# Kernel tuning notes

Hardware: AMD Instinct MI355X
Metric: run time of the kernel (lower is better)

The kernel has to match this reference:

```python
import jax, jax.numpy as jnp
import numpy as np

N_NODES = 50000
N_EDGES = 800000
D = 128


def setup_inputs() -> dict:
    key = jax.random.key(0)
    k1, k2, k3, k4, k5 = jax.random.split(key, 5)
    N = jax.random.normal(k1, (N_NODES, D), dtype=jnp.float32)
    W1 = jax.random.normal(k2, (D, D), dtype=jnp.float32) * (1.0 / np.sqrt(D))
    w2 = jax.random.normal(k3, (D,), dtype=jnp.float32) * (1.0 / np.sqrt(D))
    src = jax.random.randint(k4, (N_EDGES,), 0, N_NODES, dtype=jnp.int32)
    dst = jax.random.randint(k5, (N_EDGES,), 0, N_NODES, dtype=jnp.int32)
    return {"N": N, "W1": W1, "w2": w2, "src": src, "dst": dst}


def reference(N, W1, w2, src, dst):
    n_nodes = N.shape[0]
    # Per-node attention logit: fc2(tanh(fc1(N))). Logit depends only on the
    # source node, so compute once per node then gather per edge (same math).
    logit = jnp.tanh(N @ W1.T) @ w2            # [n_nodes]
    e = logit[src]                              # [n_edges] per-edge logit
    # Segment softmax over each destination node's incoming edges
    seg_max = jax.ops.segment_max(e, dst, num_segments=n_nodes)
    seg_max = jnp.where(jnp.isfinite(seg_max), seg_max, 0.0)  # empty segments
    ex = jnp.exp(e - seg_max[dst])              # [n_edges]
    denom = jax.ops.segment_sum(ex, dst, num_segments=n_nodes)  # [n_nodes]
    a = ex / denom[dst]                         # attention weight per edge
    # Weighted scatter-sum of gathered source features
    Np = jax.ops.segment_sum(a[:, None] * N[src], dst, num_segments=n_nodes)
    return Np
```

## Files before the change

kernel.cpp:

```cpp
#include <hip/hip_runtime.h>
#include <hip/hip_bf16.h>

#define D 128
#define NPB 16
#define CHUNK 6144
#define BKN 64
#define MAXBUCK 1024
#define NCHUNK_MAX 192
#define CAP 4096

typedef __attribute__((ext_vector_type(8))) short bf16x8;
typedef __attribute__((ext_vector_type(4))) float f32x4;

__device__ __forceinline__ unsigned short f2bf_rne(float f) {
  unsigned u = __float_as_uint(f);
  unsigned r = (u + 0x7FFFu + ((u >> 16) & 1u)) >> 16;
  return (unsigned short)r;
}

__device__ __forceinline__ float fast_tanh(float x) {
  float e = __expf(2.0f * x);
  return 1.0f - 2.0f / (e + 1.0f);
}

__device__ __forceinline__ void split8(const float* __restrict__ p,
                                       bf16x8& hv, bf16x8& lv) {
  float4 a = *(const float4*)p;
  float4 b = *(const float4*)(p + 4);
  float xs[8] = {a.x, a.y, a.z, a.w, b.x, b.y, b.z, b.w};
#pragma unroll
  for (int i = 0; i < 8; ++i) {
    unsigned short h = f2bf_rne(xs[i]);
    float hf = __uint_as_float((unsigned)h << 16);
    hv[i] = (short)h;
    lv[i] = (short)f2bf_rne(xs[i] - hf);
  }
}

struct SMLogit {
  unsigned short lhi[64 * 128];
  unsigned short llo[64 * 128];
  float part[4][64];
};
struct SMBin {
  unsigned cnt[MAXBUCK];
  unsigned cur[MAXBUCK];
  unsigned ebuf[CHUNK];
  int sdata[256];
};
union SMU {
  SMLogit lg;
  SMBin bn;
};

__global__ __launch_bounds__(256, 2) void logit_bin_kernel(
    const float* __restrict__ Nm, const float* __restrict__ W1,
    const float* __restrict__ w2, float* __restrict__ explog,
    unsigned short* __restrict__ nbf, int n_nodes,
    const int* __restrict__ src, const int* __restrict__ dst,
    unsigned* __restrict__ binout, unsigned short* __restrict__ dir,
    int n_edges, int nbuck, int nblk_bin) {
  __shared__ SMU sm;
  const int tid = threadIdx.x;

  if ((int)blockIdx.x < nblk_bin) {
    const int blk = (int)blockIdx.x;
    const int ebase = blk * CHUNK;
    const int chunkN = min(CHUNK, n_edges - ebase);

    for (int i = tid; i < MAXBUCK; i += 256) sm.bn.cnt[i] = 0;
    __syncthreads();

    for (int i = tid; i < chunkN; i += 256) {
      int d = dst[ebase + i];
      atomicAdd(&sm.bn.cnt[d >> 6], 1u);
    }
    __syncthreads();

    int t4 = tid * 4;
    int c0 = sm.bn.cnt[t4], c1 = sm.bn.cnt[t4 + 1];
    int c2 = sm.bn.cnt[t4 + 2], c3 = sm.bn.cnt[t4 + 3];
    int s = c0 + c1 + c2 + c3;
    sm.bn.sdata[tid] = s;
    __syncthreads();
    for (int d = 1; d < 256; d <<= 1) {
      int v = (tid >= d) ? sm.bn.sdata[tid - d] : 0;
      __syncthreads();
      sm.bn.sdata[tid] += v;
      __syncthreads();
    }
    int tb = sm.bn.sdata[tid] - s;
    sm.bn.cur[t4] = tb;
    sm.bn.cur[t4 + 1] = tb + c0;
    sm.bn.cur[t4 + 2] = tb + c0 + c1;
    sm.bn.cur[t4 + 3] = tb + c0 + c1 + c2;
    __syncthreads();

    size_t dbase = (size_t)blk * (nbuck + 1);
    for (int k = tid; k < nbuck; k += 256)
      dir[dbase + k] = (unsigned short)sm.bn.cur[k];
    if (tid == 0) dir[dbase + nbuck] = (unsigned short)chunkN;
    __syncthreads();

    for (int i = tid; i < chunkN; i += 256) {
      int d = dst[ebase + i];
      int sv = src[ebase + i];
      unsigned slot = atomicAdd(&sm.bn.cur[d >> 6], 1u);
      sm.bn.ebuf[slot] = (unsigned)sv | ((unsigned)(d & 63) << 16);
    }
    __syncthreads();

    for (int i = tid; i < chunkN; i += 256) binout[ebase + i] = sm.bn.ebuf[i];
  } else {
    const int w = tid >> 6;
    const int l = tid & 63;
    const int lg = l >> 4;
    const int ln = l & 15;
    const int base = ((int)blockIdx.x - nblk_bin) * 64;

    bf16x8 Bh[2][4], Bl[2][4];
#pragma unroll
    for (int ntl = 0; ntl < 2; ++ntl) {
      int n = (w * 2 + ntl) * 16 + ln;
#pragma unroll
      for (int kt = 0; kt < 4; ++kt) {
        int k = kt * 32 + lg * 8;
        split8(W1 + n * 128 + k, Bh[ntl][kt], Bl[ntl][kt]);
      }
    }

#pragma unroll
    for (int i = 0; i < 8; ++i) {
      int flat = tid + i * 256;
      int row = flat >> 5;
      int c4 = flat & 31;
      int grow = base + row;
      if (grow >= n_nodes) grow = n_nodes - 1;
      float4 v = *(const float4*)(Nm + (size_t)grow * D + c4 * 4);
      unsigned short h0 = f2bf_rne(v.x), h1 = f2bf_rne(v.y);
      unsigned short h2 = f2bf_rne(v.z), h3 = f2bf_rne(v.w);
      unsigned short o0 = f2bf_rne(v.x - __uint_as_float((unsigned)h0 << 16));
      unsigned short o1 = f2bf_rne(v.y - __uint_as_float((unsigned)h1 << 16));
      unsigned short o2 = f2bf_rne(v.z - __uint_as_float((unsigned)h2 << 16));
      unsigned short o3 = f2bf_rne(v.w - __uint_as_float((unsigned)h3 << 16));
      int boff = (c4 * 8) ^ ((row & 7) << 4);
      *(ushort4*)((char*)sm.lg.lhi + row * 256 + boff) =
          make_ushort4(h0, h1, h2, h3);
      *(ushort4*)((char*)sm.lg.llo + row * 256 + boff) =
          make_ushort4(o0, o1, o2, o3);
      *(ushort4*)(nbf + (size_t)grow * D + c4 * 4) =
          make_ushort4(h0, h1, h2, h3);
    }
    __syncthreads();

    f32x4 acc[4][2];
#pragma unroll
    for (int mt = 0; mt < 4; ++mt)
#pragma unroll
      for (int ntl = 0; ntl < 2; ++ntl)
        acc[mt][ntl] = (f32x4){0.f, 0.f, 0.f, 0.f};

#pragma unroll
    for (int mt = 0; mt < 4; ++mt) {
      int row = mt * 16 + ln;
      bf16x8 Ah[4], Al[4];
#pragma unroll
      for (int kt = 0; kt < 4; ++kt) {
        int boff = (kt * 64 + lg * 16) ^ ((row & 7) << 4);
        Ah[kt] = *(const bf16x8*)((const char*)sm.lg.lhi + row * 256 + boff);
        Al[kt] = *(const bf16x8*)((const char*)sm.lg.llo + row * 256 + boff);
      }
#pragma unroll
      for (int ntl = 0; ntl < 2; ++ntl) {
#pragma unroll
        for (int kt = 0; kt < 4; ++kt) {
          acc[mt][ntl] = __builtin_amdgcn_mfma_f32_16x16x32_bf16(
              Ah[kt], Bh[ntl][kt], acc[mt][ntl], 0, 0, 0);
          acc[mt][ntl] = __builtin_amdgcn_mfma_f32_16x16x32_bf16(
              Ah[kt], Bl[ntl][kt], acc[mt][ntl], 0, 0, 0);
          acc[mt][ntl] = __builtin_amdgcn_mfma_f32_16x16x32_bf16(
              Al[kt], Bh[ntl][kt], acc[mt][ntl], 0, 0, 0);
        }
      }
    }

    float w2a = w2[(w * 2 + 0) * 16 + ln];
    float w2b = w2[(w * 2 + 1) * 16 + ln];
#pragma unroll
    for (int mt = 0; mt < 4; ++mt) {
      float s0 =
          fast_tanh(acc[mt][0][0]) * w2a + fast_tanh(acc[mt][1][0]) * w2b;
      float s1 =
          fast_tanh(acc[mt][0][1]) * w2a + fast_tanh(acc[mt][1][1]) * w2b;
      float s2 =
          fast_tanh(acc[mt][0][2]) * w2a + fast_tanh(acc[mt][1][2]) * w2b;
      float s3 =
          fast_tanh(acc[mt][0][3]) * w2a + fast_tanh(acc[mt][1][3]) * w2b;
#pragma unroll
      for (int mask = 1; mask < 16; mask <<= 1) {
        s0 += __shfl_xor(s0, mask);
        s1 += __shfl_xor(s1, mask);
        s2 += __shfl_xor(s2, mask);
        s3 += __shfl_xor(s3, mask);
      }
      if (ln < 4) {
        float sv = (ln == 0) ? s0 : (ln == 1) ? s1 : (ln == 2) ? s2 : s3;
        sm.lg.part[w][mt * 16 + lg * 4 + ln] = sv;
      }
    }
    __syncthreads();
    if (tid < 64) {
      int node = base + tid;
      if (node < n_nodes) {
        float t = sm.lg.part[0][tid] + sm.lg.part[1][tid] +
                  sm.lg.part[2][tid] + sm.lg.part[3][tid];
        explog[node] = expf(t);
      }
    }
  }
}

__global__ __launch_bounds__(256) void merge_kernel(
    const unsigned* __restrict__ binout, const unsigned short* __restrict__ dir,
    unsigned* __restrict__ sorted, int* __restrict__ offsets,
    int* __restrict__ ends, int n_nodes, int nbuck, int nblk_bin) {
  __shared__ unsigned ebuf[CAP];
  __shared__ int lens[NCHUNK_MAX], cstart[NCHUNK_MAX], ls0[NCHUNK_MAX];
  __shared__ int cnt[BKN], nstart[BKN], cur[BKN];
  __shared__ int total;
  const int tid = threadIdx.x;
  const int w = tid >> 6, lane = tid & 63;
  const int bk = blockIdx.x;
  const int node0 = bk * BKN;
  const int base = bk * CAP;

  if (tid < nblk_bin) {
    size_t dbase = (size_t)tid * (nbuck + 1);
    int s0 = dir[dbase + bk];
    int s1 = dir[dbase + bk + 1];
    ls0[tid] = s0;
    lens[tid] = s1 - s0;
  }
  if (tid < BKN) cnt[tid] = 0;
  __syncthreads();

  if (w == 0) {
    int l0 = lane * 3, l1 = l0 + 1, l2 = l0 + 2;
    int a = (l0 < nblk_bin) ? lens[l0] : 0;
    int b = (l1 < nblk_bin) ? lens[l1] : 0;
    int c = (l2 < nblk_bin) ? lens[l2] : 0;
    int sv = a + b + c;
    int inc = sv;
#pragma unroll
    for (int off = 1; off < 64; off <<= 1) {
      int t = __shfl_up(inc, off);
      if (lane >= off) inc += t;
    }
    int ex = inc - sv;
    if (l0 < nblk_bin) cstart[l0] = ex;
    if (l1 < nblk_bin) cstart[l1] = ex + a;
    if (l2 < nblk_bin) cstart[l2] = ex + a + b;
    if (lane == 63) total = (inc > CAP) ? CAP : inc;
  }
  __syncthreads();
  const int tot = total;

  for (int r = w; r < nblk_bin; r += 4) {
    int len = lens[r], cs = cstart[r];
    if (cs >= CAP) continue;
    if (cs + len > CAP) len = CAP - cs;
    const unsigned* g = binout + (size_t)r * CHUNK + ls0[r];
    for (int i = lane; i < len; i += 64) ebuf[cs + i] = g[i];
  }
  __syncthreads();

  for (int i = tid; i < tot; i += 256) atomicAdd(&cnt[ebuf[i] >> 16], 1);
  __syncthreads();

  if (w == 0) {
    int c = cnt[lane];
    int inc = c;
#pragma unroll
    for (int off = 1; off < 64; off <<= 1) {
      int t = __shfl_up(inc, off);
      if (lane >= off) inc += t;
    }
    nstart[lane] = inc - c;
  }
  __syncthreads();

  if (tid < BKN) {
    cur[tid] = nstart[tid];
    int node = node0 + tid;
    if (node < n_nodes) {
      offsets[node] = base + nstart[tid];
      ends[node] = base + nstart[tid] + cnt[tid];
    }
  }
  __syncthreads();

  for (int i = tid; i < tot; i += 256) {
    unsigned p = ebuf[i];
    int pos = atomicAdd(&cur[p >> 16], 1);
    sorted[(size_t)base + pos] = p;
  }
}

__global__ __launch_bounds__(256) void accum_sorted_kernel(
    const int* __restrict__ offsets, const int* __restrict__ ends,
    const unsigned* __restrict__ sorted, const float* __restrict__ explog,
    const unsigned short* __restrict__ nbf, float* __restrict__ out,
    int n_nodes) {
  int node = (blockIdx.x * 256 + threadIdx.x) >> 6;
  int lane = threadIdx.x & 63;
  if (node >= n_nodes) return;
  const int eg = lane >> 4;
  const int fl = lane & 15;
  int beg = offsets[node], end = ends[node];
  int last = end - 1;
  float acc[8];
#pragma unroll
  for (int j = 0; j < 8; ++j) acc[j] = 0.f;
  float den = 0.f;

  for (int e = beg; e < end; e += 8) {
    int ea = e + eg;
    int eb = e + 4 + eg;
    int eca = (ea < last) ? ea : last;
    int ecb = (eb < last) ? eb : last;
    unsigned pa = sorted[eca];
    unsigned pb = sorted[ecb];
    int sa = pa & 0xFFFF, sb = pb & 0xFFFF;
    float xa = explog[sa];
    float xb = explog[sb];
    uint4 ua = *(const uint4*)(nbf + (size_t)sa * D + fl * 8);
    uint4 ub = *(const uint4*)(nbf + (size_t)sb * D + fl * 8);
    xa = (ea < end) ? xa : 0.f;
    xb = (eb < end) ? xb : 0.f;
    den += xa + xb;
    unsigned va[4] = {ua.x, ua.y, ua.z, ua.w};
    unsigned vb[4] = {ub.x, ub.y, ub.z, ub.w};
#pragma unroll
    for (int j = 0; j < 4; ++j) {
      acc[2 * j] += xa * __uint_as_float(va[j] << 16) +
                    xb * __uint_as_float(vb[j] << 16);
      acc[2 * j + 1] += xa * __uint_as_float(va[j] & 0xFFFF0000u) +
                        xb * __uint_as_float(vb[j] & 0xFFFF0000u);
    }
  }

#pragma unroll
  for (int j = 0; j < 8; ++j) {
    acc[j] += __shfl_xor(acc[j], 16);
    acc[j] += __shfl_xor(acc[j], 32);
  }
  den += __shfl_xor(den, 16);
  den += __shfl_xor(den, 32);

  if (eg == 0) {
    float inv = (end > beg) ? 1.0f / den : 0.f;
    float4 o0 = make_float4(acc[0] * inv, acc[1] * inv, acc[2] * inv,
                            acc[3] * inv);
    float4 o1 = make_float4(acc[4] * inv, acc[5] * inv, acc[6] * inv,
                            acc[7] * inv);
    float* orow = out + (size_t)node * D + fl * 8;
    *(float4*)orow = o0;
    *(float4*)(orow + 4) = o1;
  }
}

__global__ __launch_bounds__(256) void logit_kernel(
    const float* __restrict__ Nm, const float* __restrict__ W1,
    const float* __restrict__ w2, float* __restrict__ logit, int n_nodes) {
  __shared__ float w1t[32 * 129];
  const int tid = threadIdx.x;
  const int j = tid & 127;
  const int half = tid >> 7;
  const int base = blockIdx.x * NPB;
  float acc[8];
#pragma unroll
  for (int g = 0; g < 8; ++g) acc[g] = 0.f;
  for (int c = 0; c < 4; ++c) {
    __syncthreads();
    for (int idx = tid; idx < 128 * 32; idx += 256) {
      int kl = idx & 31, jj = idx >> 5;
      w1t[kl * 129 + jj] = W1[jj * 128 + c * 32 + kl];
    }
    __syncthreads();
#pragma unroll
    for (int g = 0; g < 8; ++g) {
      int node = base + g * 2 + half;
      if (node < n_nodes) {
        const float4* nrow =
            reinterpret_cast<const float4*>(Nm + (size_t)node * D + c * 32);
        float a = acc[g];
#pragma unroll
        for (int k4 = 0; k4 < 8; ++k4) {
          float4 nv = nrow[k4];
          int kl = k4 * 4;
          a += nv.x * w1t[(kl + 0) * 129 + j];
          a += nv.y * w1t[(kl + 1) * 129 + j];
          a += nv.z * w1t[(kl + 2) * 129 + j];
          a += nv.w * w1t[(kl + 3) * 129 + j];
        }
        acc[g] = a;
      }
    }
  }
  const float w2j = w2[j];
#pragma unroll
  for (int g = 0; g < 8; ++g) {
    int node = base + g * 2 + half;
    float t = tanhf(acc[g]) * w2j;
#pragma unroll
    for (int off = 32; off; off >>= 1) t += __shfl_down(t, off);
    if ((tid & 63) == 0 && node < n_nodes) atomicAdd(&logit[node], t);
  }
}

__global__ __launch_bounds__(256) void denom_kernel(
    const int* __restrict__ src, const int* __restrict__ dst,
    const float* __restrict__ logit, float* __restrict__ denom, int n_edges) {
  int e = blockIdx.x * 256 + threadIdx.x;
  if (e < n_edges) {
    float ex = expf(logit[src[e]]);
    atomicAdd(&denom[dst[e]], ex);
  }
}

__global__ __launch_bounds__(256) void scatter_kernel(
    const int* __restrict__ src, const int* __restrict__ dst,
    const float* __restrict__ logit, const float* __restrict__ denom,
    const float* __restrict__ Nm, float* __restrict__ out, int n_edges) {
  int wave = (blockIdx.x * 256 + threadIdx.x) >> 6;
  int lane = threadIdx.x & 63;
  if (wave >= n_edges) return;
  int s = src[wave];
  int d = dst[wave];
  float a = expf(logit[s]) / denom[d];
  float v0 = Nm[(size_t)s * D + lane];
  float v1 = Nm[(size_t)s * D + 64 + lane];
  atomicAdd(&out[(size_t)d * D + lane], a * v0);
  atomicAdd(&out[(size_t)d * D + 64 + lane], a * v1);
}

static inline char* align_up(char* p, size_t a) {
  return (char*)(((uintptr_t)p + a - 1) & ~(uintptr_t)(a - 1));
}

extern "C" void kernel_launch(void* const* d_in, const int* in_sizes, int n_in,
                              void* d_out, int out_size, void* d_ws,
                              size_t ws_size, hipStream_t stream) {
  const float* Nm  = (const float*)d_in[0];
  const float* W1  = (const float*)d_in[1];
  const float* w2  = (const float*)d_in[2];
  const int*   src = (const int*)d_in[3];
  const int*   dst = (const int*)d_in[4];
  float* out = (float*)d_out;

  const int n_nodes = in_sizes[0] / D;
  const int n_edges = in_sizes[3];
  const int n_pad = (n_nodes + 63) & ~63;
  const int nbuck = (n_nodes + BKN - 1) / BKN;
  const int nblk_bin = (n_edges + CHUNK - 1) / CHUNK;

  char* p = (char*)d_ws;
  float* explog = (float*)p;     p = align_up(p + (size_t)n_pad * 4, 256);
  float* denomF = (float*)p;     p = align_up(p + (size_t)n_pad * 4, 256);
  unsigned short* nbf = (unsigned short*)p;
  p = align_up(p + (size_t)n_nodes * D * 2, 256);
  unsigned* binout = (unsigned*)p;
  p = align_up(p + (size_t)nblk_bin * CHUNK * 4, 256);
  unsigned short* dir = (unsigned short*)p;
  p = align_up(p + (size_t)nblk_bin * (nbuck + 1) * 2, 256);
  unsigned* sorted = (unsigned*)p;
  p = align_up(p + (size_t)nbuck * CAP * 4, 256);
  int* offsets = (int*)p;        p = align_up(p + (size_t)n_pad * 4, 256);
  int* ends    = (int*)p;        p = align_up(p + (size_t)n_pad * 4, 256);
  size_t needed = (size_t)(p - (char*)d_ws);

  const bool fits = (ws_size >= needed) && (n_nodes <= 65535) &&
                    (nbuck <= MAXBUCK) && (nblk_bin <= NCHUNK_MAX) &&
                    ((n_edges / (nbuck > 0 ? nbuck : 1)) * 3 < CAP);

  if (fits) {
    int nblk1 = (n_nodes + 63) / 64;
    logit_bin_kernel<<<nblk_bin + nblk1, 256, 0, stream>>>(
        Nm, W1, w2, explog, nbf, n_nodes, src, dst, binout, dir, n_edges,
        nbuck, nblk_bin);

    merge_kernel<<<nbuck, 256, 0, stream>>>(binout, dir, sorted, offsets,
                                            ends, n_nodes, nbuck, nblk_bin);

    int ablk = (n_nodes + 3) / 4;
    accum_sorted_kernel<<<ablk, 256, 0, stream>>>(
        offsets, ends, sorted, explog, nbf, out, n_nodes);
  } else {
    float* logit = explog;
    float* denom = denomF;
    hipMemsetAsync(logit, 0, (size_t)n_pad * sizeof(float), stream);
    hipMemsetAsync(denom, 0, (size_t)n_pad * sizeof(float), stream);
    hipMemsetAsync(out, 0, (size_t)out_size * sizeof(float), stream);
    int nblk1 = (n_nodes + NPB - 1) / NPB;
    logit_kernel<<<nblk1, 256, 0, stream>>>(Nm, W1, w2, logit, n_nodes);
    int eblk = (n_edges + 255) / 256;
    denom_kernel<<<eblk, 256, 0, stream>>>(src, dst, logit, denom, n_edges);
    int nblk3 = (n_edges + 3) / 4;
    scatter_kernel<<<nblk3, 256, 0, stream>>>(src, dst, logit, denom, Nm, out,
                                              n_edges);
  }
}
```

Baseline: 81.35 us.

## Shrink binning chunks, truncate bf16 hi split, and gather edge runs with 8-lane groups

Reduces CHUNK from 6144 to 3584 and raises NCHUNK_MAX to 256, so more binning blocks run and the per-bucket prefix scan now handles four entries per lane. The bf16 hi/lo split of N and W1 now takes the hi part by plain truncation instead of round-to-nearest, and the lo part absorbs the larger residual. The gather of per-bucket edge runs now gives each run an 8-lane group instead of a whole wavefront, which suits the shorter runs. Truncation slightly changes the split-precision rounding, and the smaller chunks give each bucket more, shorter runs to merge.

New measurement: 67.46 us. 1.21x faster.

```diff
diff --git a/kernel.cpp b/kernel.cpp
--- a/kernel.cpp
+++ b/kernel.cpp
@@ -3,10 +3,10 @@
 
 #define D 128
 #define NPB 16
-#define CHUNK 6144
+#define CHUNK 3584
 #define BKN 64
 #define MAXBUCK 1024
-#define NCHUNK_MAX 192
+#define NCHUNK_MAX 256
 #define CAP 4096
 
 typedef __attribute__((ext_vector_type(8))) short bf16x8;
@@ -30,10 +30,10 @@
   float xs[8] = {a.x, a.y, a.z, a.w, b.x, b.y, b.z, b.w};
 #pragma unroll
   for (int i = 0; i < 8; ++i) {
-    unsigned short h = f2bf_rne(xs[i]);
-    float hf = __uint_as_float((unsigned)h << 16);
-    hv[i] = (short)h;
-    lv[i] = (short)f2bf_rne(xs[i] - hf);
+    unsigned u = __float_as_uint(xs[i]);
+    hv[i] = (short)(u >> 16);
+    float r = xs[i] - __uint_as_float(u & 0xFFFF0000u);
+    lv[i] = (short)f2bf_rne(r);
   }
 }
 
@@ -137,12 +137,16 @@
       int grow = base + row;
       if (grow >= n_nodes) grow = n_nodes - 1;
       float4 v = *(const float4*)(Nm + (size_t)grow * D + c4 * 4);
-      unsigned short h0 = f2bf_rne(v.x), h1 = f2bf_rne(v.y);
-      unsigned short h2 = f2bf_rne(v.z), h3 = f2bf_rne(v.w);
-      unsigned short o0 = f2bf_rne(v.x - __uint_as_float((unsigned)h0 << 16));
-      unsigned short o1 = f2bf_rne(v.y - __uint_as_float((unsigned)h1 << 16));
-      unsigned short o2 = f2bf_rne(v.z - __uint_as_float((unsigned)h2 << 16));
-      unsigned short o3 = f2bf_rne(v.w - __uint_as_float((unsigned)h3 << 16));
+      unsigned ux = __float_as_uint(v.x), uy = __float_as_uint(v.y);
+      unsigned uz = __float_as_uint(v.z), uw = __float_as_uint(v.w);
+      unsigned short h0 = (unsigned short)(ux >> 16);
+      unsigned short h1 = (unsigned short)(uy >> 16);
+      unsigned short h2 = (unsigned short)(uz >> 16);
+      unsigned short h3 = (unsigned short)(uw >> 16);
+      unsigned short o0 = f2bf_rne(v.x - __uint_as_float(ux & 0xFFFF0000u));
+      unsigned short o1 = f2bf_rne(v.y - __uint_as_float(uy & 0xFFFF0000u));
+      unsigned short o2 = f2bf_rne(v.z - __uint_as_float(uz & 0xFFFF0000u));
+      unsigned short o3 = f2bf_rne(v.w - __uint_as_float(uw & 0xFFFF0000u));
       int boff = (c4 * 8) ^ ((row & 7) << 4);
       *(ushort4*)((char*)sm.lg.lhi + row * 256 + boff) =
           make_ushort4(h0, h1, h2, h3);
@@ -245,11 +249,12 @@
   __syncthreads();
 
   if (w == 0) {
-    int l0 = lane * 3, l1 = l0 + 1, l2 = l0 + 2;
-    int a = (l0 < nblk_bin) ? lens[l0] : 0;
-    int b = (l1 < nblk_bin) ? lens[l1] : 0;
-    int c = (l2 < nblk_bin) ? lens[l2] : 0;
-    int sv = a + b + c;
+    int l0 = lane * 4;
+    int a = (l0 + 0 < nblk_bin) ? lens[l0 + 0] : 0;
+    int b = (l0 + 1 < nblk_bin) ? lens[l0 + 1] : 0;
+    int c = (l0 + 2 < nblk_bin) ? lens[l0 + 2] : 0;
+    int d = (l0 + 3 < nblk_bin) ? lens[l0 + 3] : 0;
+    int sv = a + b + c + d;
     int inc = sv;
 #pragma unroll
     for (int off = 1; off < 64; off <<= 1) {
@@ -257,20 +262,25 @@
       if (lane >= off) inc += t;
     }
     int ex = inc - sv;
-    if (l0 < nblk_bin) cstart[l0] = ex;
-    if (l1 < nblk_bin) cstart[l1] = ex + a;
-    if (l2 < nblk_bin) cstart[l2] = ex + a + b;
+    if (l0 + 0 < nblk_bin) cstart[l0 + 0] = ex;
+    if (l0 + 1 < nblk_bin) cstart[l0 + 1] = ex + a;
+    if (l0 + 2 < nblk_bin) cstart[l0 + 2] = ex + a + b;
+    if (l0 + 3 < nblk_bin) cstart[l0 + 3] = ex + a + b + c;
     if (lane == 63) total = (inc > CAP) ? CAP : inc;
   }
   __syncthreads();
   const int tot = total;
 
-  for (int r = w; r < nblk_bin; r += 4) {
-    int len = lens[r], cs = cstart[r];
-    if (cs >= CAP) continue;
-    if (cs + len > CAP) len = CAP - cs;
-    const unsigned* g = binout + (size_t)r * CHUNK + ls0[r];
-    for (int i = lane; i < len; i += 64) ebuf[cs + i] = g[i];
+  {
+    const int rg = lane >> 3;
+    const int li = lane & 7;
+    for (int r = w * 8 + rg; r < nblk_bin; r += 32) {
+      int len = lens[r], cs = cstart[r];
+      if (cs >= CAP) continue;
+      if (cs + len > CAP) len = CAP - cs;
+      const unsigned* g = binout + (size_t)r * CHUNK + ls0[r];
+      for (int i = li; i < len; i += 8) ebuf[cs + i] = g[i];
+    }
   }
   __syncthreads();
 
```
